# Optimization experiments

Hardware: AMD Instinct MI355X
Metric: run time of the kernel (lower is better)

## Reference

```python
import jax, jax.numpy as jnp
import numpy as np

G, N, F = 16, 2048, 32          # graphs, nodes/graph, node feature width
E = 32768                        # edges per graph (avg degree 16)
INPUT_DIM = N * F                # 65536, matches reshape in original forward
H, L = 512, 64                   # VAE hidden width, latent dim
BN_EPS = 1e-5
NEG_SLOPE = 0.01                 # nn.LeakyReLU default


def setup_inputs() -> dict:
    key = jax.random.key(0)
    ks = jax.random.split(key, 18)
    f32 = jnp.float32
    inp = {
        "x": jax.random.normal(ks[0], (G, N, F), dtype=f32),
        "edge_index": jax.random.randint(ks[1], (G, 2, E), 0, N, dtype=jnp.int32),
        "eps": jax.random.normal(ks[2], (G, L), dtype=f32),
        # GCNConv weight + bias
        "W_gcn": jax.random.normal(ks[3], (F, F), dtype=f32) / np.sqrt(F),
        "b_gcn": jnp.zeros((F,), dtype=f32),
        # BatchNorm1d(num_features) affine params
        "bn_gamma": jnp.ones((F,), dtype=f32),
        "bn_beta": jnp.zeros((F,), dtype=f32),
        # VAE encoder trunk + mean / log_var heads
        "W_enc": jax.random.normal(ks[4], (INPUT_DIM, H), dtype=f32) / np.sqrt(INPUT_DIM),
        "b_enc": jnp.zeros((H,), dtype=f32),
        "W_mu": jax.random.normal(ks[5], (H, L), dtype=f32) / np.sqrt(H),
        "b_mu": jnp.zeros((L,), dtype=f32),
        "W_lv": jax.random.normal(ks[6], (H, L), dtype=f32) / np.sqrt(H),
        "b_lv": jnp.zeros((L,), dtype=f32),
        # VAE decoder
        "W_dec1": jax.random.normal(ks[7], (L, H), dtype=f32) / np.sqrt(L),
        "b_dec1": jnp.zeros((H,), dtype=f32),
        "W_dec2": jax.random.normal(ks[8], (H, INPUT_DIM), dtype=f32) / np.sqrt(H),
        "b_dec2": jnp.zeros((INPUT_DIM,), dtype=f32),
    }
    return inp


def _gcn_conv(xg, eig, W_gcn, b_gcn):
    # PyG GCNConv: add self-loops, symmetric normalization D^-1/2 A D^-1/2
    src, dst = eig[0], eig[1]
    loop = jnp.arange(N, dtype=src.dtype)
    src = jnp.concatenate([src, loop])
    dst = jnp.concatenate([dst, loop])
    deg = jax.ops.segment_sum(jnp.ones(src.shape, dtype=xg.dtype), dst, num_segments=N)
    dinv = jax.lax.rsqrt(deg)  # deg >= 1 due to self-loops
    xw = xg @ W_gcn                                  # [N, F]
    coef = dinv[src] * dinv[dst]                     # [E+N]
    msg = xw[src] * coef[:, None]                    # gather + scale
    return jax.ops.segment_sum(msg, dst, num_segments=N) + b_gcn  # scatter-add


def reference(x, edge_index, eps, W_gcn, b_gcn, bn_gamma, bn_beta,
              W_enc, b_enc, W_mu, b_mu, W_lv, b_lv,
              W_dec1, b_dec1, W_dec2, b_dec2):
    # convolute(): per-graph GCN conv -> BatchNorm1d (batch stats over that graph's
    # nodes) -> tanh -> dropout (identity in eval) -> concat. Vectorized via vmap.
    h = jax.vmap(_gcn_conv, in_axes=(0, 0, None, None))(x, edge_index, W_gcn, b_gcn)  # [G,N,F]
    mu_n = h.mean(axis=1, keepdims=True)
    var_n = h.var(axis=1, keepdims=True)  # biased variance, as torch BN uses in normalization
    h = (h - mu_n) * jax.lax.rsqrt(var_n + BN_EPS) * bn_gamma + bn_beta
    h = jnp.tanh(h)
    xs = h.reshape(G, INPUT_DIM)
    # VariationalExample forward
    henc = jax.nn.leaky_relu(xs @ W_enc + b_enc, NEG_SLOPE)   # [G, H]
    mean = henc @ W_mu + b_mu                                  # [G, L]
    log_var = henc @ W_lv + b_lv                               # [G, L]
    z = mean + jnp.exp(0.5 * log_var) * eps                    # reparameterize
    hd = jax.nn.leaky_relu(z @ W_dec1 + b_dec1, NEG_SLOPE)     # [G, H]
    x_hat = hd @ W_dec2 + b_dec2                               # [G, INPUT_DIM]
    return x_hat, mean, log_var
```

## Files before the change

kernel.cpp:

```cpp
#include <hip/hip_runtime.h>
#include <hip/hip_bf16.h>

#define NG 16
#define NN 2048
#define NF 32
#define NE 32768
#define IND 65536
#define HD 512
#define LD 64

typedef unsigned int u32;


__global__ void k_zerodeg(float4* __restrict__ p){
  p[blockIdx.x * 256 + threadIdx.x] = make_float4(0.f, 0.f, 0.f, 0.f);
}

__global__ void k_xwdeg(const float* __restrict__ x, const float* __restrict__ Wg,
                        float* __restrict__ xw, const int* __restrict__ ei,
                        u32* __restrict__ deg, u32* __restrict__ pos){
  int t = threadIdx.x;
  int bid = blockIdx.x;
  if (bid < 4096){
    __shared__ float ws[32][33];
    __shared__ float xsh[8][32];
    for (int i = t; i < 1024; i += 256) ws[i >> 5][i & 31] = Wg[i];
    int base = bid * 8;
    int r = t >> 5, f = t & 31;
    xsh[r][f] = x[(base + r) * 32 + f];
    __syncthreads();
    float acc = 0.f;
    #pragma unroll
    for (int k = 0; k < 32; ++k) acc += xsh[r][k] * ws[k][f];
    xw[(base + r) * 32 + f] = acc;
  } else {
    __shared__ u32 hist[2048];
    __shared__ u32 basesh[2048];
    int db = bid - 4096;
    int g = db >> 2, chunk = db & 3;
    int e0 = chunk * 8192;
    const int* dstp = ei + (g * 2 + 1) * NE + e0;
    for (int i = t; i < 2048; i += 256) hist[i] = 0u;
    __syncthreads();
    #pragma unroll
    for (int j = 0; j < 32; ++j)
      atomicAdd(&hist[dstp[j * 256 + t]], 1u);
    __syncthreads();
    for (int n = t; n < 2048; n += 256)
      basesh[n] = atomicAdd(&deg[g * NN + n], hist[n]);
    __syncthreads();
    for (int n = t; n < 2048; n += 256) hist[n] = 0u;
    __syncthreads();
    #pragma unroll
    for (int j = 0; j < 32; ++j){
      int e = j * 256 + t;
      int dst = dstp[e];
      u32 loc = atomicAdd(&hist[dst], 1u);
      pos[g * NE + e0 + e] = basesh[dst] + loc;
    }
  }
}

__global__ void k_prefix(const u32* __restrict__ deg, u32* __restrict__ offs,
                         float* __restrict__ dinv){
  int g = blockIdx.x, t = threadIdx.x;
  const u32* dg = deg + g * NN;
  u32 loc[8]; u32 s = 0;
  #pragma unroll
  for (int i = 0; i < 8; ++i){ loc[i] = s; s += dg[t * 8 + i]; }
  __shared__ u32 bs[256];
  bs[t] = s; __syncthreads();
  for (int d = 1; d < 256; d <<= 1){
    u32 v = (t >= d) ? bs[t - d] : 0u;
    __syncthreads();
    bs[t] += v;
    __syncthreads();
  }
  u32 base = bs[t] - s;
  #pragma unroll
  for (int i = 0; i < 8; ++i){
    int n = t * 8 + i;
    offs[g * NN + n] = g * NE + base + loc[i];
    dinv[g * NN + n] = rsqrtf((float)(dg[n] + 1u));
  }
}

__global__ void k_sortedges(const int* __restrict__ ei, const u32* __restrict__ offs,
                            const u32* __restrict__ pos, u32* __restrict__ sorted){
  int idx = blockIdx.x * 256 + threadIdx.x;
  int g = idx >> 15, e = idx & (NE - 1);
  int src = ei[g * 2 * NE + e];
  int dst = ei[(g * 2 + 1) * NE + e];
  sorted[offs[g * NN + dst] + pos[idx]] = (u32)src;
}

__global__ void k_gather(const u32* __restrict__ sorted, const u32* __restrict__ offs,
                         const u32* __restrict__ deg, const float* __restrict__ dinv,
                         const float* __restrict__ xw, const float* __restrict__ bg,
                         float* __restrict__ h){
  int tid = blockIdx.x * 256 + threadIdx.x;
  int q = tid & 7, n = (tid >> 3) & (NN - 1), g = tid >> 14;
  int gn = g * NN + n;
  u32 o0 = offs[gn];
  u32 cnt = deg[gn];
  float dn = dinv[gn];
  const float4* xw4 = (const float4*)xw;
  float4 acc = make_float4(0.f, 0.f, 0.f, 0.f);
  for (u32 e = 0; e < cnt; ++e){
    u32 src = sorted[o0 + e];
    float c = dinv[g * NN + src] * dn;
    float4 v = xw4[(size_t)(g * NN + src) * 8 + q];
    acc.x += c * v.x; acc.y += c * v.y; acc.z += c * v.z; acc.w += c * v.w;
  }
  float c2 = dn * dn;
  float4 v = xw4[(size_t)gn * 8 + q];
  float4 b = ((const float4*)bg)[q];
  acc.x += c2 * v.x + b.x; acc.y += c2 * v.y + b.y;
  acc.z += c2 * v.z + b.z; acc.w += c2 * v.w + b.w;
  ((float4*)h)[(size_t)gn * 8 + q] = acc;
}


__global__ void k_bnstat(const float* __restrict__ h, float* __restrict__ pstat){
  int g = blockIdx.x >> 3, s = blockIdx.x & 7;
  int t = threadIdx.x, f = t & 31, r = t >> 5;
  float s1 = 0.f, s2 = 0.f;
  for (int it = 0; it < 32; ++it){
    int n = s * 256 + it * 8 + r;
    float v = h[(size_t)(g * NN + n) * 32 + f];
    s1 += v; s2 += v * v;
  }
  __shared__ float l1[256], l2[256];
  l1[t] = s1; l2[t] = s2;
  __syncthreads();
  if (t < 32){
    float a = 0.f, b = 0.f;
    #pragma unroll
    for (int r2 = 0; r2 < 8; ++r2){ a += l1[r2 * 32 + t]; b += l2[r2 * 32 + t]; }
    pstat[((g * 8 + s) * 32 + t) * 2 + 0] = a;
    pstat[((g * 8 + s) * 32 + t) * 2 + 1] = b;
  }
}


__global__ __launch_bounds__(256) void k_gemvenc(const float* __restrict__ h,
    const float* __restrict__ pstat, const float* __restrict__ gamma,
    const float* __restrict__ beta, const float* __restrict__ B,
    float* __restrict__ part){
  __shared__ float ash[64 * 16];
  __shared__ float ssc[512], ssh[512];
  int t = threadIdx.x;
  int k0 = blockIdx.x * 64;
  for (int i = t; i < 512; i += 256){
    int g = i >> 5, f = i & 31;
    float s1 = 0.f, s2 = 0.f;
    #pragma unroll
    for (int s = 0; s < 8; ++s){
      s1 += pstat[((g * 8 + s) * 32 + f) * 2 + 0];
      s2 += pstat[((g * 8 + s) * 32 + f) * 2 + 1];
    }
    float mean = s1 * (1.f / NN);
    float var  = s2 * (1.f / NN) - mean * mean;
    float sc = gamma[f] * rsqrtf(var + 1e-5f);
    ssc[i] = sc;
    ssh[i] = beta[f] - mean * sc;
  }
  __syncthreads();
  for (int idx = t; idx < 1024; idx += 256){
    int i = idx & 63, g = idx >> 6;
    int f = i & 31;
    float v = h[(size_t)g * IND + k0 + i];
    ash[i * 16 + g] = tanhf(v * ssc[g * 32 + f] + ssh[g * 32 + f]);
  }
  __syncthreads();
  float acc[32];
  #pragma unroll
  for (int i = 0; i < 32; ++i) acc[i] = 0.f;
  const float2* bp = (const float2*)(B + (size_t)k0 * 512) + t;
  for (int kk = 0; kk < 64; kk += 8){
    float2 bv[8];
    #pragma unroll
    for (int u = 0; u < 8; ++u) bv[u] = bp[(size_t)(kk + u) * 256];
    #pragma unroll
    for (int u = 0; u < 8; ++u){
      const float* ap = &ash[(kk + u) * 16];
      #pragma unroll
      for (int m = 0; m < 16; ++m){
        acc[2*m]   += ap[m] * bv[u].x;
        acc[2*m+1] += ap[m] * bv[u].y;
      }
    }
  }
  float* pp = part + (size_t)blockIdx.x * 8192 + t * 2;
  #pragma unroll
  for (int m = 0; m < 16; ++m)
    *(float2*)(pp + (size_t)m * 512) = make_float2(acc[2*m], acc[2*m+1]);
}

__global__ void k_encred1(const float* __restrict__ part, float* __restrict__ p2){
  int idx = blockIdx.x * 256 + threadIdx.x;
  int out = idx & 8191, grp = idx >> 13;
  const float* p = part + (size_t)grp * 128 * 8192 + out;
  float s = 0.f;
  #pragma unroll 8
  for (int c = 0; c < 128; ++c) s += p[(size_t)c * 8192];
  p2[idx] = s;
}

__global__ __launch_bounds__(512) void k_headdec(const float* __restrict__ p2,
    const float* __restrict__ be,
    const float* __restrict__ Wmu, const float* __restrict__ bmu,
    const float* __restrict__ Wlv, const float* __restrict__ blv,
    const float* __restrict__ eps, const float* __restrict__ W1,
    const float* __restrict__ b1, float* __restrict__ hdT, float* __restrict__ outp){
  int g = blockIdx.x, t = threadIdx.x;
  __shared__ float hsh[512];
  __shared__ float zsh[64];
  float hv = be[t];
  #pragma unroll
  for (int grp = 0; grp < 8; ++grp) hv += p2[grp * 8192 + g * 512 + t];
  hv = hv > 0.f ? hv : 0.01f * hv;
  hsh[t] = hv;
  __syncthreads();
  int l = t >> 3, r = t & 7;
  float am = 0.f, av = 0.f;
  for (int k = r; k < 512; k += 8){
    float hh = hsh[k];
    am += hh * Wmu[k * 64 + l];
    av += hh * Wlv[k * 64 + l];
  }
  #pragma unroll
  for (int d = 1; d < 8; d <<= 1){
    am += __shfl_xor(am, d);
    av += __shfl_xor(av, d);
  }
  if (r == 0){
    float mean = am + bmu[l];
    float lv   = av + blv[l];
    float z = mean + expf(0.5f * lv) * eps[g * 64 + l];
    zsh[l] = z;
    outp[1048576 + g * 64 + l] = mean;
    outp[1049600 + g * 64 + l] = lv;
  }
  __syncthreads();
  float a = 0.f;
  #pragma unroll
  for (int k = 0; k < 64; ++k) a += zsh[k] * W1[k * 512 + t];
  a += b1[t];
  a = a > 0.f ? a : 0.01f * a;
  hdT[t * 16 + g] = a;
}


__global__ __launch_bounds__(256) void k_gemvdec(const float* __restrict__ A,
                          const float* __restrict__ B,
                          const float* __restrict__ bias,
                          float* __restrict__ outp){
  __shared__ float ash[8192];
  int t = threadIdx.x;
  int nt = blockIdx.x;
  for (int i = t; i < 8192; i += 256) ash[i] = A[i];
  __syncthreads();
  int cp = t & 31;
  int kq = t >> 5;
  float acc[32];
  #pragma unroll
  for (int i = 0; i < 32; ++i) acc[i] = 0.f;
  const float2* bp = (const float2*)B + (size_t)(kq * 64) * 32768 + nt * 32 + cp;
  for (int kk = 0; kk < 64; kk += 8){
    float2 bv[8];
    #pragma unroll
    for (int u = 0; u < 8; ++u) bv[u] = bp[(size_t)(kk + u) * 32768];
    #pragma unroll
    for (int u = 0; u < 8; ++u){
      const float* ap = &ash[(kq * 64 + kk + u) * 16];
      #pragma unroll
      for (int m = 0; m < 16; ++m){
        acc[2*m]   += ap[m] * bv[u].x;
        acc[2*m+1] += ap[m] * bv[u].y;
      }
    }
  }
  __syncthreads();
  #pragma unroll
  for (int m = 0; m < 16; ++m){
    ash[kq * 1024 + (m * 2 + 0) * 32 + cp] = acc[2*m];
    ash[kq * 1024 + (m * 2 + 1) * 32 + cp] = acc[2*m+1];
  }
  __syncthreads();
  #pragma unroll
  for (int jj = 0; jj < 2; ++jj){
    int idx = t * 2 + jj;
    int m = idx >> 5, c = idx & 31;
    float sx = 0.f, sy = 0.f;
    #pragma unroll
    for (int q = 0; q < 8; ++q){
      sx += ash[q * 1024 + (m * 2 + 0) * 32 + c];
      sy += ash[q * 1024 + (m * 2 + 1) * 32 + c];
    }
    float2 bb = ((const float2*)bias)[nt * 32 + c];
    *(float2*)(outp + (size_t)m * 65536 + nt * 64 + c * 2) =
        make_float2(sx + bb.x, sy + bb.y);
  }
}


extern "C" void kernel_launch(void* const* d_in, const int* in_sizes, int n_in,
                              void* d_out, int out_size, void* d_ws, size_t ws_size,
                              hipStream_t stream){
  const float* x     = (const float*)d_in[0];
  const int*   ei    = (const int*)d_in[1];
  const float* eps   = (const float*)d_in[2];
  const float* Wg    = (const float*)d_in[3];
  const float* bg    = (const float*)d_in[4];
  const float* gamma = (const float*)d_in[5];
  const float* beta  = (const float*)d_in[6];
  const float* Wenc  = (const float*)d_in[7];
  const float* benc  = (const float*)d_in[8];
  const float* Wmu   = (const float*)d_in[9];
  const float* bmu   = (const float*)d_in[10];
  const float* Wlv   = (const float*)d_in[11];
  const float* blv   = (const float*)d_in[12];
  const float* Wd1   = (const float*)d_in[13];
  const float* bd1   = (const float*)d_in[14];
  const float* Wd2   = (const float*)d_in[15];
  const float* bd2   = (const float*)d_in[16];
  float* outp = (float*)d_out;

  char* ws = (char*)d_ws;
  const size_t OFF_XW     = 0;
  const size_t OFF_H      = 4194304;
  const size_t OFF_DEG    = 8388608;
  const size_t OFF_DINV   = 8519680;
  const size_t OFF_PSTAT  = 8650752;
  const size_t OFF_HDT    = 8683520;
  const size_t OFF_P2     = 8716288;
  const size_t OFF_POS    = 8978432;
  const size_t OFF_PART   = 11075584;
  const size_t OFF_SORT   = OFF_PART;
  const size_t OFF_OFFS   = OFF_PART + 2097152;

  float* xw     = (float*)(ws + OFF_XW);
  float* h      = (float*)(ws + OFF_H);
  u32*   deg    = (u32*)  (ws + OFF_DEG);
  float* dinv   = (float*)(ws + OFF_DINV);
  float* pstat  = (float*)(ws + OFF_PSTAT);
  float* hdT    = (float*)(ws + OFF_HDT);
  float* p2     = (float*)(ws + OFF_P2);
  u32*   pos    = (u32*)  (ws + OFF_POS);
  float* part   = (float*)(ws + OFF_PART);
  u32*   sorted = (u32*)  (ws + OFF_SORT);
  u32*   offs   = (u32*)  (ws + OFF_OFFS);

  k_zerodeg  <<<32,   256, 0, stream>>>((float4*)(ws + OFF_DEG));
  k_xwdeg    <<<4160, 256, 0, stream>>>(x, Wg, xw, ei, deg, pos);
  k_prefix   <<<16,   256, 0, stream>>>(deg, offs, dinv);
  k_sortedges<<<2048, 256, 0, stream>>>(ei, offs, pos, sorted);
  k_gather   <<<1024, 256, 0, stream>>>(sorted, offs, deg, dinv, xw, bg, h);
  k_bnstat   <<<128,  256, 0, stream>>>(h, pstat);

  k_gemvenc  <<<1024, 256, 0, stream>>>(h, pstat, gamma, beta, Wenc, part);
  k_encred1  <<<256,  256, 0, stream>>>(part, p2);

  k_headdec  <<<16, 512, 0, stream>>>(p2, benc, Wmu, bmu, Wlv, blv, eps, Wd1, bd1, hdT, outp);

  k_gemvdec  <<<1024, 256, 0, stream>>>(hdT, Wd2, bd2, outp);
}
```

Measured before the change: 159.4 us.

## Replace global degree atomics with per-chunk histograms and prefetch encoder weights into cache

Each edge chunk now writes its local destination histogram to a buffer instead of atomically adding into a global degree array. The prefix kernel sums the four chunk histograms and emits per-chunk base offsets, which removes the zeroing kernel and the global atomics. Extra blocks are also appended to the xw/degree kernel and the gather kernel. They read the 128 MB encoder weight matrix (W_enc) and discard the result, so it sits in cache for the later encoder GEMV. This adds traffic to the early kernels, and only part of W_enc can stay resident in the last-level cache.

```diff
diff --git a/kernel.cpp b/kernel.cpp
--- a/kernel.cpp
+++ b/kernel.cpp
@@ -12,13 +12,10 @@
 typedef unsigned int u32;
 
 
-__global__ void k_zerodeg(float4* __restrict__ p){
-  p[blockIdx.x * 256 + threadIdx.x] = make_float4(0.f, 0.f, 0.f, 0.f);
-}
-
 __global__ void k_xwdeg(const float* __restrict__ x, const float* __restrict__ Wg,
                         float* __restrict__ xw, const int* __restrict__ ei,
-                        u32* __restrict__ deg, u32* __restrict__ pos){
+                        u32* __restrict__ hist4, u32* __restrict__ pos,
+                        const float* __restrict__ Wenc){
   int t = threadIdx.x;
   int bid = blockIdx.x;
   if (bid < 4096){
@@ -33,9 +30,8 @@
     #pragma unroll
     for (int k = 0; k < 32; ++k) acc += xsh[r][k] * ws[k][f];
     xw[(base + r) * 32 + f] = acc;
-  } else {
+  } else if (bid < 4160){
     __shared__ u32 hist[2048];
-    __shared__ u32 basesh[2048];
     int db = bid - 4096;
     int g = db >> 2, chunk = db & 3;
     int e0 = chunk * 8192;
@@ -46,28 +42,44 @@
     for (int j = 0; j < 32; ++j)
       atomicAdd(&hist[dstp[j * 256 + t]], 1u);
     __syncthreads();
-    for (int n = t; n < 2048; n += 256)
-      basesh[n] = atomicAdd(&deg[g * NN + n], hist[n]);
-    __syncthreads();
-    for (int n = t; n < 2048; n += 256) hist[n] = 0u;
+    for (int n = t; n < 2048; n += 256){
+      u32 v = hist[n];
+      hist4[db * 2048 + n] = v;
+      hist[n] = 0u;
+    }
     __syncthreads();
     #pragma unroll
     for (int j = 0; j < 32; ++j){
       int e = j * 256 + t;
       int dst = dstp[e];
       u32 loc = atomicAdd(&hist[dst], 1u);
-      pos[g * NE + e0 + e] = basesh[dst] + loc;
-    }
-  }
-}
-
-__global__ void k_prefix(const u32* __restrict__ deg, u32* __restrict__ offs,
-                         float* __restrict__ dinv){
+      pos[g * NE + e0 + e] = loc;
+    }
+  } else {
+    int pb = bid - 4160;
+    const float4* p = (const float4*)Wenc + (size_t)pb * 2048 + t;
+    float acc = 0.f;
+    #pragma unroll
+    for (int j = 0; j < 8; ++j){
+      float4 v = p[j * 256];
+      acc += v.x + v.y + v.z + v.w;
+    }
+    asm volatile("" :: "v"(acc));
+  }
+}
+
+__global__ void k_prefix(const u32* __restrict__ hist4, u32* __restrict__ offs,
+                         u32* __restrict__ deg, float* __restrict__ dinv,
+                         u32* __restrict__ basech){
   int g = blockIdx.x, t = threadIdx.x;
-  const u32* dg = deg + g * NN;
   u32 loc[8]; u32 s = 0;
   #pragma unroll
-  for (int i = 0; i < 8; ++i){ loc[i] = s; s += dg[t * 8 + i]; }
+  for (int i = 0; i < 8; ++i){
+    int n = t * 8 + i;
+    u32 d = hist4[(g * 4 + 0) * 2048 + n] + hist4[(g * 4 + 1) * 2048 + n]
+          + hist4[(g * 4 + 2) * 2048 + n] + hist4[(g * 4 + 3) * 2048 + n];
+    loc[i] = s; s += d;
+  }
   __shared__ u32 bs[256];
   bs[t] = s; __syncthreads();
   for (int d = 1; d < 256; d <<= 1){
@@ -80,25 +92,51 @@
   #pragma unroll
   for (int i = 0; i < 8; ++i){
     int n = t * 8 + i;
-    offs[g * NN + n] = g * NE + base + loc[i];
-    dinv[g * NN + n] = rsqrtf((float)(dg[n] + 1u));
-  }
-}
-
-__global__ void k_sortedges(const int* __restrict__ ei, const u32* __restrict__ offs,
+    u32 h0 = hist4[(g * 4 + 0) * 2048 + n];
+    u32 h1 = hist4[(g * 4 + 1) * 2048 + n];
+    u32 h2 = hist4[(g * 4 + 2) * 2048 + n];
+    u32 h3 = hist4[(g * 4 + 3) * 2048 + n];
+    u32 d = h0 + h1 + h2 + h3;
+    u32 o = g * NE + base + loc[i];
+    offs[g * NN + n] = o;
+    deg [g * NN + n] = d;
+    dinv[g * NN + n] = rsqrtf((float)(d + 1u));
+    basech[(g * 4 + 0) * 2048 + n] = o;
+    basech[(g * 4 + 1) * 2048 + n] = o + h0;
+    basech[(g * 4 + 2) * 2048 + n] = o + h0 + h1;
+    basech[(g * 4 + 3) * 2048 + n] = o + h0 + h1 + h2;
+  }
+}
+
+__global__ void k_sortedges(const int* __restrict__ ei, const u32* __restrict__ basech,
                             const u32* __restrict__ pos, u32* __restrict__ sorted){
   int idx = blockIdx.x * 256 + threadIdx.x;
   int g = idx >> 15, e = idx & (NE - 1);
+  int chunk = e >> 13;
   int src = ei[g * 2 * NE + e];
   int dst = ei[(g * 2 + 1) * NE + e];
-  sorted[offs[g * NN + dst] + pos[idx]] = (u32)src;
+  sorted[basech[(g * 4 + chunk) * 2048 + dst] + pos[idx]] = (u32)src;
 }
 
 __global__ void k_gather(const u32* __restrict__ sorted, const u32* __restrict__ offs,
                          const u32* __restrict__ deg, const float* __restrict__ dinv,
                          const float* __restrict__ xw, const float* __restrict__ bg,
-                         float* __restrict__ h){
-  int tid = blockIdx.x * 256 + threadIdx.x;
+                         float* __restrict__ h, const float* __restrict__ Wenc){
+  int t = threadIdx.x;
+  int bid = blockIdx.x;
+  if (bid >= 1024){
+    int pb = bid - 1024;
+    const float4* p = (const float4*)Wenc + (size_t)(2048 + pb) * 2048 + t;
+    float acc = 0.f;
+    #pragma unroll
+    for (int j = 0; j < 8; ++j){
+      float4 v = p[j * 256];
+      acc += v.x + v.y + v.z + v.w;
+    }
+    asm volatile("" :: "v"(acc));
+    return;
+  }
+  int tid = bid * 256 + t;
   int q = tid & 7, n = (tid >> 3) & (NN - 1), g = tid >> 14;
   int gn = g * NN + n;
   u32 o0 = offs[gn];
@@ -336,7 +374,9 @@
   const size_t OFF_HDT    = 8683520;
   const size_t OFF_P2     = 8716288;
   const size_t OFF_POS    = 8978432;
-  const size_t OFF_PART   = 11075584;
+  const size_t OFF_HIST4  = 11075584;
+  const size_t OFF_BASECH = 11599872;
+  const size_t OFF_PART   = 12124160;
   const size_t OFF_SORT   = OFF_PART;
   const size_t OFF_OFFS   = OFF_PART + 2097152;
 
@@ -348,15 +388,16 @@
   float* hdT    = (float*)(ws + OFF_HDT);
   float* p2     = (float*)(ws + OFF_P2);
   u32*   pos    = (u32*)  (ws + OFF_POS);
+  u32*   hist4  = (u32*)  (ws + OFF_HIST4);
+  u32*   basech = (u32*)  (ws + OFF_BASECH);
   float* part   = (float*)(ws + OFF_PART);
   u32*   sorted = (u32*)  (ws + OFF_SORT);
   u32*   offs   = (u32*)  (ws + OFF_OFFS);
 
-  k_zerodeg  <<<32,   256, 0, stream>>>((float4*)(ws + OFF_DEG));
-  k_xwdeg    <<<4160, 256, 0, stream>>>(x, Wg, xw, ei, deg, pos);
-  k_prefix   <<<16,   256, 0, stream>>>(deg, offs, dinv);
-  k_sortedges<<<2048, 256, 0, stream>>>(ei, offs, pos, sorted);
-  k_gather   <<<1024, 256, 0, stream>>>(sorted, offs, deg, dinv, xw, bg, h);
+  k_xwdeg    <<<6208, 256, 0, stream>>>(x, Wg, xw, ei, hist4, pos, Wenc);
+  k_prefix   <<<16,   256, 0, stream>>>(hist4, offs, deg, dinv, basech);
+  k_sortedges<<<2048, 256, 0, stream>>>(ei, basech, pos, sorted);
+  k_gather   <<<3072, 256, 0, stream>>>(sorted, offs, deg, dinv, xw, bg, h, Wenc);
   k_bnstat   <<<128,  256, 0, stream>>>(h, pstat);
 
   k_gemvenc  <<<1024, 256, 0, stream>>>(h, pstat, gamma, beta, Wenc, part);
```

Result: slower. 181.0 us (+13.6%).
